# Kernel optimization log

Measured on AMD Instinct MI355X. Metric: run time of the kernel, lower is better.

## Reference

```python
import jax, jax.numpy as jnp
import numpy as np

B_SZ, IN_DIM, N_NEURONS, N_LAYERS, N_OUTS = 65536, 4, 512, 8, 4


def setup_inputs() -> dict:
    key = jax.random.key(0)
    ks = jax.random.split(key, 5)
    glorot = lambda k, shape: jax.random.normal(k, shape, jnp.float32) * np.sqrt(2.0 / (shape[-2] + shape[-1]))
    inputs = jax.random.normal(ks[0], (B_SZ, IN_DIM), jnp.float32)
    # GaussianRFF projection matrix (fixed random Gaussian)
    B_rff = jax.random.normal(ks[1], (IN_DIM, N_NEURONS // 2), jnp.float32)
    Ws = glorot(ks[2], (N_LAYERS, N_NEURONS, N_NEURONS))
    bs = jnp.zeros((N_LAYERS, N_NEURONS), jnp.float32)
    alphas = jnp.zeros((N_LAYERS + 1,), jnp.float32)  # LAAF slopes, init 0
    Wf = glorot(ks[3], (N_NEURONS, N_OUTS))           # final mixer, no bias
    scale = jnp.ones((N_OUTS,), jnp.float32)          # Scaler, no bias
    return {"inputs": inputs, "B_rff": B_rff, "Ws": Ws, "bs": bs,
            "alphas": alphas, "Wf": Wf, "scale": scale}


def _mlp(x, B_rff, Ws, bs, alphas, Wf, scale):
    # Gaussian random Fourier feature embedding -> [B, n_neurons]
    z = x @ B_rff
    u = jnp.concatenate([jnp.sin(z), jnp.cos(z)], axis=-1)
    L = Ws.shape[0]
    def step(u, p):
        W, b, a = p
        # LAAF sine layer: sin(w0 * (1 + alpha) * (uW + b)), w0 = 1.0
        return jnp.sin((1.0 + a) * (u @ W + b)), None
    u, _ = jax.lax.scan(step, u, (Ws, bs, alphas[:L]))
    return (u @ Wf) * scale  # [B, 4] = (A1, A2, A3, phi)


def reference(inputs, B_rff, Ws, bs, alphas, Wf, scale):
    f = lambda x: _mlp(x, B_rff, Ws, bs, alphas, Wf, scale)
    def jvp_col(col):
        tang = jnp.zeros_like(inputs).at[:, col].set(1.0)
        return jax.jvp(f, (inputs,), (tang,))
    # input columns: 0=t, 1=z, 2=x, 3=y
    P, dPdz = jvp_col(1)
    _, dPdx = jvp_col(2)
    _, dPdy = jvp_col(3)
    A1_y, A1_z = dPdy[:, 0:1], dPdz[:, 0:1]
    A2_x, A2_z = dPdx[:, 1:2], dPdz[:, 1:2]
    A3_x, A3_y = dPdx[:, 2:3], dPdy[:, 2:3]
    phi_x, phi_y, phi_z = dPdx[:, 3:4], dPdy[:, 3:4], dPdz[:, 3:4]
    u = (A3_y - A2_z) + phi_x
    v = (A1_z - A3_x) + phi_y
    w = (A2_x - A1_y) + phi_z
    return jnp.concatenate([u, v, w], axis=1)
```

## Files before the change

### kernel.cpp

```cpp
#include <hip/hip_runtime.h>
#include <stdint.h>


#define B_SZ   65536
#define NN     512
#define NL     8
#define SPB    24
#define MROWS  96
#define MT     6
#define NTW    4
#define NKB    16
#define KB_BYTES 32768
#define LDS_A  (MROWS*1024)
#define LDS_TOTAL (LDS_A + 2*KB_BYTES)

typedef _Float16 f16x8 __attribute__((ext_vector_type(8)));
typedef float    f32x4 __attribute__((ext_vector_type(4)));

__device__ __forceinline__ uint16_t f2h_bits(float f) {
  union { _Float16 h; uint16_t u; } v; v.h = (_Float16)f; return v.u;
}
__device__ __forceinline__ float h2f(uint16_t b) {
  union { uint16_t u; _Float16 h; } v; v.u = b; return (float)v.h;
}

__global__ __launch_bounds__(512) void prep_weights(const float* __restrict__ Ws,
                                                    uint16_t* __restrict__ img) {
  const int n  = threadIdx.x;
  const int kb = blockIdx.x & 15;
  const int l  = blockIdx.x >> 4;
  const float* src = Ws + ((size_t)l << 18) + n;
  char* dstbase = (char*)img + (((size_t)(l*16 + kb)) << 15) + (size_t)n * 64;
  #pragma unroll
  for (int kq = 0; kq < 4; ++kq) {
    uint16_t h[8];
    #pragma unroll
    for (int e = 0; e < 8; ++e) {
      int k = kb*32 + kq*8 + e;
      h[e] = f2h_bits(src[(size_t)k * 512]);
    }
    uint4 pk;
    pk.x = (uint32_t)h[0] | ((uint32_t)h[1] << 16);
    pk.y = (uint32_t)h[2] | ((uint32_t)h[3] << 16);
    pk.z = (uint32_t)h[4] | ((uint32_t)h[5] << 16);
    pk.w = (uint32_t)h[6] | ((uint32_t)h[7] << 16);
    *(uint4*)(dstbase + 16 * ((kq + (n >> 1)) & 3)) = pk;
  }
}

__global__ __launch_bounds__(512, 2) void pinn_fused(
    const float* __restrict__ inputs, const float* __restrict__ Brff,
    const float* __restrict__ bs, const float* __restrict__ alphas,
    const float* __restrict__ Wf, const float* __restrict__ scl,
    const uint16_t* __restrict__ wimg, float* __restrict__ out)
{
  extern __shared__ char smem[];
  char* wbuf0 = smem + LDS_A;
  char* wbuf1 = smem + LDS_A + KB_BYTES;

  const int tid  = threadIdx.x;
  const int lane = tid & 63;
  const int wv   = tid >> 6;
  const int i16  = lane & 15;
  const int q    = lane >> 4;
  const int sbase = blockIdx.x * SPB;

  float* brff = (float*)wbuf0;
  brff[tid]       = Brff[tid];
  brff[tid + 512] = Brff[tid + 512];
  __syncthreads();

  {
    const int k = tid;
    const int col = k & 255;
    const bool iscos = (k >= 256);
    const float b0 = brff[col], b1 = brff[256 + col], b2 = brff[512 + col], b3 = brff[768 + col];
    for (int m = 0; m < MROWS; ++m) {
      int s = sbase + (m >> 2); if (s >= B_SZ) s = B_SZ - 1;
      const int stream = m & 3;
      const float* x = inputs + (size_t)s * 4;
      float z = x[0]*b0 + x[1]*b1 + x[2]*b2 + x[3]*b3;
      float szn = __sinf(z), czn = __cosf(z);
      float val;
      if (stream == 0) val = iscos ? czn : szn;
      else {
        float bc = (stream == 1) ? b1 : (stream == 2 ? b2 : b3);
        val = iscos ? (-szn * bc) : (czn * bc);
      }
      *(uint16_t*)(smem + m*1024 + ((2*k) ^ ((m & 7) * 16))) = f2h_bits(val);
    }
  }
  __syncthreads();

  auto stage = [&](int g, char* buf) {
    const char* src = (const char*)wimg + ((size_t)g << 15) + (size_t)(wv*4) * 1024 + (size_t)lane * 16;
    char* dst = buf + (wv*4) * 1024;
    #pragma unroll
    for (int it = 0; it < 4; ++it) {
      __builtin_amdgcn_global_load_lds(
          (const __attribute__((address_space(1))) void*)(src + it*1024),
          (__attribute__((address_space(3))) void*)(dst + it*1024),
          16, 0, 0);
    }
  };

  stage(0, wbuf0);
  __syncthreads();

  f32x4 acc[MT][NTW];

  for (int l = 0; l < NL; ++l) {
    const f32x4 zz = {0.f, 0.f, 0.f, 0.f};
    #pragma unroll
    for (int a = 0; a < MT; ++a)
      #pragma unroll
      for (int b = 0; b < NTW; ++b)
        acc[a][b] = zz;

    for (int kb = 0; kb < NKB; ++kb) {
      const int g = l*NKB + kb;
      char* cur = (g & 1) ? wbuf1 : wbuf0;
      if (g + 1 < NL*NKB) stage(g + 1, (g & 1) ? wbuf0 : wbuf1);

      f16x8 af[MT];
      #pragma unroll
      for (int Mt = 0; Mt < MT; ++Mt) {
        const int m = Mt*16 + i16;
        af[Mt] = *(const f16x8*)(smem + m*1024 + ((kb*64 + q*16) ^ ((i16 & 7) * 16)));
      }
      f16x8 bfr[NTW];
      #pragma unroll
      for (int Nt = 0; Nt < NTW; ++Nt) {
        const int nc = wv*64 + Nt*16 + i16;
        bfr[Nt] = *(const f16x8*)(cur + nc*64 + 16 * ((q + (nc >> 1)) & 3));
      }
      #pragma unroll
      for (int Mt = 0; Mt < MT; ++Mt)
        #pragma unroll
        for (int Nt = 0; Nt < NTW; ++Nt)
          acc[Mt][Nt] = __builtin_amdgcn_mfma_f32_16x16x32_f16(af[Mt], bfr[Nt], acc[Mt][Nt], 0, 0, 0);
      __syncthreads();
    }

    const float opa = 1.0f + alphas[l];
    #pragma unroll
    for (int Nt = 0; Nt < NTW; ++Nt) {
      const int nc = wv*64 + Nt*16 + i16;
      const float bias = bs[l*NN + nc];
      #pragma unroll
      for (int Mt = 0; Mt < MT; ++Mt) {
        f32x4 c = acc[Mt][Nt];
        float h  = opa * (c[0] + bias);
        float un = __sinf(h);
        float fc = opa * __cosf(h);
        float vv[4] = { un, fc*c[1], fc*c[2], fc*c[3] };
        const int mb = Mt*16 + q*4;
        #pragma unroll
        for (int r = 0; r < 4; ++r) {
          const int m = mb + r;
          *(uint16_t*)(smem + m*1024 + ((2*nc) ^ ((m & 7) * 16))) = f2h_bits(vv[r]);
        }
      }
    }
    __syncthreads();
  }

  float* dp = (float*)wbuf0;
  const float4 sc4 = *(const float4*)scl;
  for (int rr = 0; rr < MROWS/8; ++rr) {
    const int m = wv * 12 + rr;
    float p0 = 0.f, p1 = 0.f, p2 = 0.f, p3 = 0.f;
    #pragma unroll
    for (int j = 0; j < 8; ++j) {
      const int k = lane + j*64;
      float a = h2f(*(const uint16_t*)(smem + m*1024 + ((2*k) ^ ((m & 7) * 16))));
      float4 wf = ((const float4*)Wf)[k];
      p0 += a*wf.x; p1 += a*wf.y; p2 += a*wf.z; p3 += a*wf.w;
    }
    #pragma unroll
    for (int d = 1; d < 64; d <<= 1) {
      p0 += __shfl_xor(p0, d, 64);
      p1 += __shfl_xor(p1, d, 64);
      p2 += __shfl_xor(p2, d, 64);
      p3 += __shfl_xor(p3, d, 64);
    }
    if (lane == 0) {
      float4* o = (float4*)(dp + m*4);
      *o = make_float4(p0*sc4.x, p1*sc4.y, p2*sc4.z, p3*sc4.w);
    }
  }
  __syncthreads();

  if (tid < SPB*3) {
    const int sl = tid / 3, c = tid - sl*3;
    const int s = sbase + sl;
    if (s < B_SZ) {
      const float* d1 = dp + (sl*4 + 1)*4;
      const float* d2 = dp + (sl*4 + 2)*4;
      const float* d3 = dp + (sl*4 + 3)*4;
      float val;
      if (c == 0)      val = d3[2] - d1[1] + d2[3];
      else if (c == 1) val = d1[0] - d2[2] + d3[3];
      else             val = d2[1] - d3[0] + d1[3];
      out[(size_t)s*3 + c] = val;
    }
  }
}

extern "C" void kernel_launch(void* const* d_in, const int* in_sizes, int n_in,
                              void* d_out, int out_size, void* d_ws, size_t ws_size,
                              hipStream_t stream) {
  const float* inputs = (const float*)d_in[0];
  const float* Brff   = (const float*)d_in[1];
  const float* Ws     = (const float*)d_in[2];
  const float* bsp    = (const float*)d_in[3];
  const float* alph   = (const float*)d_in[4];
  const float* Wfp    = (const float*)d_in[5];
  const float* sclp   = (const float*)d_in[6];
  uint16_t* wimg = (uint16_t*)d_ws;

  prep_weights<<<NL*NKB/2 * 2 , 512, 0, stream>>>(Ws, wimg);
  const int nblocks = (B_SZ + SPB - 1) / SPB;
  pinn_fused<<<nblocks, 512, LDS_TOTAL, stream>>>(inputs, Brff, bsp, alph, Wfp, sclp,
                                                  wimg, (float*)d_out);
}
```

Measured before the change: 1.430 ms.

## Load weight fragments directly into registers, shrink tile for higher occupancy

Weights are no longer staged through double-buffered LDS. prep_weights now lays them out in MFMA fragment order so each wave reads its B fragments straight from global memory (L2) into registers, with register double buffering across k-blocks. This removes the per-k-block __syncthreads and the 64KB of weight LDS. Samples per block drop from 24 to 16 and launch bounds go to 4 blocks/CU, trading weight reuse per block for more occupancy and more L2 traffic. The RFF embedding is also computed per sample, with one sin/cos shared across its four tangent rows.

```diff
diff --git a/kernel.cpp b/kernel.cpp
--- a/kernel.cpp
+++ b/kernel.cpp
@@ -5,14 +5,14 @@
 #define B_SZ   65536
 #define NN     512
 #define NL     8
-#define SPB    24
-#define MROWS  96
-#define MT     6
+#define SPB    16
+#define MROWS  64
+#define MT     4
 #define NTW    4
 #define NKB    16
-#define KB_BYTES 32768
+#define NG     (NL*NKB)
 #define LDS_A  (MROWS*1024)
-#define LDS_TOTAL (LDS_A + 2*KB_BYTES)
+#define LDS_TOTAL (LDS_A + 1024)
 
 typedef _Float16 f16x8 __attribute__((ext_vector_type(8)));
 typedef float    f32x4 __attribute__((ext_vector_type(4)));
@@ -26,37 +26,36 @@
 
 __global__ __launch_bounds__(512) void prep_weights(const float* __restrict__ Ws,
                                                     uint16_t* __restrict__ img) {
-  const int n  = threadIdx.x;
-  const int kb = blockIdx.x & 15;
-  const int l  = blockIdx.x >> 4;
-  const float* src = Ws + ((size_t)l << 18) + n;
-  char* dstbase = (char*)img + (((size_t)(l*16 + kb)) << 15) + (size_t)n * 64;
+  const int g  = blockIdx.x;
+  const int l  = g >> 4, kb = g & 15;
+  const float* src = Ws + ((size_t)l << 18);
+  char* dst = (char*)img + ((size_t)g << 15);
   #pragma unroll
-  for (int kq = 0; kq < 4; ++kq) {
+  for (int it = 0; it < 4; ++it) {
+    const int fidx = threadIdx.x + it*512;
+    const int ln  = fidx & 63, sub = fidx >> 6;
+    const int n     = (sub >> 2)*64 + (sub & 3)*16 + (ln & 15);
+    const int kbase = kb*32 + (ln >> 4)*8;
     uint16_t h[8];
     #pragma unroll
-    for (int e = 0; e < 8; ++e) {
-      int k = kb*32 + kq*8 + e;
-      h[e] = f2h_bits(src[(size_t)k * 512]);
-    }
+    for (int e = 0; e < 8; ++e)
+      h[e] = f2h_bits(src[(size_t)(kbase + e)*512 + n]);
     uint4 pk;
     pk.x = (uint32_t)h[0] | ((uint32_t)h[1] << 16);
     pk.y = (uint32_t)h[2] | ((uint32_t)h[3] << 16);
     pk.z = (uint32_t)h[4] | ((uint32_t)h[5] << 16);
     pk.w = (uint32_t)h[6] | ((uint32_t)h[7] << 16);
-    *(uint4*)(dstbase + 16 * ((kq + (n >> 1)) & 3)) = pk;
-  }
-}
-
-__global__ __launch_bounds__(512, 2) void pinn_fused(
+    *(uint4*)(dst + (size_t)fidx*16) = pk;
+  }
+}
+
+__global__ __launch_bounds__(512, 4) void pinn_fused(
     const float* __restrict__ inputs, const float* __restrict__ Brff,
     const float* __restrict__ bs, const float* __restrict__ alphas,
     const float* __restrict__ Wf, const float* __restrict__ scl,
     const uint16_t* __restrict__ wimg, float* __restrict__ out)
 {
   extern __shared__ char smem[];
-  char* wbuf0 = smem + LDS_A;
-  char* wbuf1 = smem + LDS_A + KB_BYTES;
 
   const int tid  = threadIdx.x;
   const int lane = tid & 63;
@@ -65,47 +64,35 @@
   const int q    = lane >> 4;
   const int sbase = blockIdx.x * SPB;
 
-  float* brff = (float*)wbuf0;
-  brff[tid]       = Brff[tid];
-  brff[tid + 512] = Brff[tid + 512];
+  {
+    const int k = tid, col = k & 255;
+    const bool iscos = (k >= 256);
+    const float b0 = Brff[col];
+    const float b1 = Brff[256 + col];
+    const float b2 = Brff[512 + col];
+    const float b3 = Brff[768 + col];
+    const int koff = 2*k;
+    for (int s = 0; s < SPB; ++s) {
+      const float4 x = *(const float4*)(inputs + ((size_t)(sbase + s) << 2));
+      const float z = x.x*b0 + x.y*b1 + x.z*b2 + x.w*b3;
+      const float szn = __sinf(z), czn = __cosf(z);
+      const float u0 = iscos ? czn : szn;
+      const float dz = iscos ? -szn : czn;
+      const int m0 = 4*s;
+      *(uint16_t*)(smem + (size_t)(m0+0)*1024 + (koff ^ (((m0+0) & 7)*16))) = f2h_bits(u0);
+      *(uint16_t*)(smem + (size_t)(m0+1)*1024 + (koff ^ (((m0+1) & 7)*16))) = f2h_bits(dz*b1);
+      *(uint16_t*)(smem + (size_t)(m0+2)*1024 + (koff ^ (((m0+2) & 7)*16))) = f2h_bits(dz*b2);
+      *(uint16_t*)(smem + (size_t)(m0+3)*1024 + (koff ^ (((m0+3) & 7)*16))) = f2h_bits(dz*b3);
+    }
+  }
   __syncthreads();
 
-  {
-    const int k = tid;
-    const int col = k & 255;
-    const bool iscos = (k >= 256);
-    const float b0 = brff[col], b1 = brff[256 + col], b2 = brff[512 + col], b3 = brff[768 + col];
-    for (int m = 0; m < MROWS; ++m) {
-      int s = sbase + (m >> 2); if (s >= B_SZ) s = B_SZ - 1;
-      const int stream = m & 3;
-      const float* x = inputs + (size_t)s * 4;
-      float z = x[0]*b0 + x[1]*b1 + x[2]*b2 + x[3]*b3;
-      float szn = __sinf(z), czn = __cosf(z);
-      float val;
-      if (stream == 0) val = iscos ? czn : szn;
-      else {
-        float bc = (stream == 1) ? b1 : (stream == 2 ? b2 : b3);
-        val = iscos ? (-szn * bc) : (czn * bc);
-      }
-      *(uint16_t*)(smem + m*1024 + ((2*k) ^ ((m & 7) * 16))) = f2h_bits(val);
-    }
-  }
-  __syncthreads();
-
-  auto stage = [&](int g, char* buf) {
-    const char* src = (const char*)wimg + ((size_t)g << 15) + (size_t)(wv*4) * 1024 + (size_t)lane * 16;
-    char* dst = buf + (wv*4) * 1024;
-    #pragma unroll
-    for (int it = 0; it < 4; ++it) {
-      __builtin_amdgcn_global_load_lds(
-          (const __attribute__((address_space(1))) void*)(src + it*1024),
-          (__attribute__((address_space(3))) void*)(dst + it*1024),
-          16, 0, 0);
-    }
-  };
-
-  stage(0, wbuf0);
-  __syncthreads();
+  const char* wbase = (const char*)wimg + ((size_t)wv << 12) + (size_t)lane*16;
+
+  f16x8 bA[NTW], bB[NTW];
+  #pragma unroll
+  for (int Nt = 0; Nt < NTW; ++Nt)
+    bA[Nt] = *(const f16x8*)(wbase + (size_t)Nt*1024);
 
   f32x4 acc[MT][NTW];
 
@@ -114,33 +101,45 @@
     #pragma unroll
     for (int a = 0; a < MT; ++a)
       #pragma unroll
-      for (int b = 0; b < NTW; ++b)
-        acc[a][b] = zz;
-
-    for (int kb = 0; kb < NKB; ++kb) {
-      const int g = l*NKB + kb;
-      char* cur = (g & 1) ? wbuf1 : wbuf0;
-      if (g + 1 < NL*NKB) stage(g + 1, (g & 1) ? wbuf0 : wbuf1);
-
-      f16x8 af[MT];
-      #pragma unroll
-      for (int Mt = 0; Mt < MT; ++Mt) {
-        const int m = Mt*16 + i16;
-        af[Mt] = *(const f16x8*)(smem + m*1024 + ((kb*64 + q*16) ^ ((i16 & 7) * 16)));
-      }
-      f16x8 bfr[NTW];
-      #pragma unroll
-      for (int Nt = 0; Nt < NTW; ++Nt) {
-        const int nc = wv*64 + Nt*16 + i16;
-        bfr[Nt] = *(const f16x8*)(cur + nc*64 + 16 * ((q + (nc >> 1)) & 3));
-      }
-      #pragma unroll
-      for (int Mt = 0; Mt < MT; ++Mt)
-        #pragma unroll
-        for (int Nt = 0; Nt < NTW; ++Nt)
-          acc[Mt][Nt] = __builtin_amdgcn_mfma_f32_16x16x32_f16(af[Mt], bfr[Nt], acc[Mt][Nt], 0, 0, 0);
-      __syncthreads();
-    }
+      for (int b = 0; b < NTW; ++b) acc[a][b] = zz;
+
+    #pragma unroll 1
+    for (int t = 0; t < NKB/2; ++t) {
+      const int g = l*NKB + 2*t;
+      {
+        const char* p = wbase + ((size_t)(g + 1) << 15);
+        #pragma unroll
+        for (int Nt = 0; Nt < NTW; ++Nt) bB[Nt] = *(const f16x8*)(p + (size_t)Nt*1024);
+      }
+      {
+        const int kb = 2*t;
+        const int roff = (kb*64 + q*16) ^ ((i16 & 7)*16);
+        #pragma unroll
+        for (int Mt = 0; Mt < MT; ++Mt) {
+          const f16x8 af = *(const f16x8*)(smem + (size_t)(Mt*16 + i16)*1024 + roff);
+          #pragma unroll
+          for (int Nt = 0; Nt < NTW; ++Nt)
+            acc[Mt][Nt] = __builtin_amdgcn_mfma_f32_16x16x32_f16(af, bA[Nt], acc[Mt][Nt], 0, 0, 0);
+        }
+      }
+      if (g + 2 < NG) {
+        const char* p = wbase + ((size_t)(g + 2) << 15);
+        #pragma unroll
+        for (int Nt = 0; Nt < NTW; ++Nt) bA[Nt] = *(const f16x8*)(p + (size_t)Nt*1024);
+      }
+      {
+        const int kb = 2*t + 1;
+        const int roff = (kb*64 + q*16) ^ ((i16 & 7)*16);
+        #pragma unroll
+        for (int Mt = 0; Mt < MT; ++Mt) {
+          const f16x8 af = *(const f16x8*)(smem + (size_t)(Mt*16 + i16)*1024 + roff);
+          #pragma unroll
+          for (int Nt = 0; Nt < NTW; ++Nt)
+            acc[Mt][Nt] = __builtin_amdgcn_mfma_f32_16x16x32_f16(af, bB[Nt], acc[Mt][Nt], 0, 0, 0);
+        }
+      }
+    }
+    __syncthreads();
 
     const float opa = 1.0f + alphas[l];
     #pragma unroll
@@ -158,22 +157,22 @@
         #pragma unroll
         for (int r = 0; r < 4; ++r) {
           const int m = mb + r;
-          *(uint16_t*)(smem + m*1024 + ((2*nc) ^ ((m & 7) * 16))) = f2h_bits(vv[r]);
+          *(uint16_t*)(smem + (size_t)m*1024 + ((2*nc) ^ ((m & 7)*16))) = f2h_bits(vv[r]);
         }
       }
     }
     __syncthreads();
   }
 
-  float* dp = (float*)wbuf0;
+  float* dp = (float*)(smem + LDS_A);
   const float4 sc4 = *(const float4*)scl;
   for (int rr = 0; rr < MROWS/8; ++rr) {
-    const int m = wv * 12 + rr;
+    const int m = wv*(MROWS/8) + rr;
     float p0 = 0.f, p1 = 0.f, p2 = 0.f, p3 = 0.f;
     #pragma unroll
     for (int j = 0; j < 8; ++j) {
       const int k = lane + j*64;
-      float a = h2f(*(const uint16_t*)(smem + m*1024 + ((2*k) ^ ((m & 7) * 16))));
+      float a = h2f(*(const uint16_t*)(smem + (size_t)m*1024 + ((2*k) ^ ((m & 7)*16))));
       float4 wf = ((const float4*)Wf)[k];
       p0 += a*wf.x; p1 += a*wf.y; p2 += a*wf.z; p3 += a*wf.w;
     }
@@ -193,17 +192,14 @@
 
   if (tid < SPB*3) {
     const int sl = tid / 3, c = tid - sl*3;
-    const int s = sbase + sl;
-    if (s < B_SZ) {
-      const float* d1 = dp + (sl*4 + 1)*4;
-      const float* d2 = dp + (sl*4 + 2)*4;
-      const float* d3 = dp + (sl*4 + 3)*4;
-      float val;
-      if (c == 0)      val = d3[2] - d1[1] + d2[3];
-      else if (c == 1) val = d1[0] - d2[2] + d3[3];
-      else             val = d2[1] - d3[0] + d1[3];
-      out[(size_t)s*3 + c] = val;
-    }
+    const float* d1 = dp + (sl*4 + 1)*4;
+    const float* d2 = dp + (sl*4 + 2)*4;
+    const float* d3 = dp + (sl*4 + 3)*4;
+    float val;
+    if (c == 0)      val = d3[2] - d1[1] + d2[3];
+    else if (c == 1) val = d1[0] - d2[2] + d3[3];
+    else             val = d2[1] - d3[0] + d1[3];
+    out[(size_t)(sbase + sl)*3 + c] = val;
   }
 }
 
@@ -219,8 +215,8 @@
   const float* sclp   = (const float*)d_in[6];
   uint16_t* wimg = (uint16_t*)d_ws;
 
-  prep_weights<<<NL*NKB/2 * 2 , 512, 0, stream>>>(Ws, wimg);
-  const int nblocks = (B_SZ + SPB - 1) / SPB;
+  prep_weights<<<NG, 512, 0, stream>>>(Ws, wimg);
+  const int nblocks = B_SZ / SPB;
   pinn_fused<<<nblocks, 512, LDS_TOTAL, stream>>>(inputs, Brff, bsp, alph, Wfp, sclp,
                                                   wimg, (float*)d_out);
 }
```

New measurement: 1.415 ms. Within noise of the previous version (-1.1%).
